# Kernel tuning notes

Hardware: AMD Instinct MI355X
Metric: run time of the kernel (lower is better)

The kernel has to match this reference:

```python
import jax, jax.numpy as jnp
import numpy as np
from jax import lax

B, S, H, T = 64, 512, 768, 9


def setup_inputs() -> dict:
    key = jax.random.key(0)
    ks = jax.random.split(key, 7)
    hidden = jax.random.normal(ks[0], (B, S, H), dtype=jnp.float32)
    W = jax.random.normal(ks[1], (H, T), dtype=jnp.float32) * 0.02
    b = jax.random.normal(ks[2], (T,), dtype=jnp.float32) * 0.02
    start_trans = jax.random.normal(ks[3], (T,), dtype=jnp.float32) * 0.1
    end_trans = jax.random.normal(ks[4], (T,), dtype=jnp.float32) * 0.1
    trans = jax.random.normal(ks[5], (T, T), dtype=jnp.float32) * 0.1
    labels = jax.random.randint(ks[6], (B, S), 0, T, dtype=jnp.int64)
    return {"hidden": hidden, "W": W, "b": b, "start_trans": start_trans,
            "end_trans": end_trans, "trans": trans, "labels": labels}


def _crf_nll(emissions, labels, start_trans, end_trans, trans):
    # emissions: [B,S,T], labels: [B,S] int. mask = labels > -1 (torchcrf semantics).
    maskf = (labels > -1).astype(emissions.dtype)          # [B,S]
    tags = jnp.maximum(labels, 0)                          # safe indexing

    # ---- numerator: score of the gold path ----
    tags0 = tags[:, 0]                                     # [B]
    num0 = start_trans[tags0] + jnp.take_along_axis(emissions[:, 0], tags0[:, None], axis=1)[:, 0]

    em_t = jnp.swapaxes(emissions[:, 1:], 0, 1)            # [S-1,B,T]
    tg_t = jnp.swapaxes(tags[:, 1:], 0, 1)                 # [S-1,B]
    mk_t = jnp.swapaxes(maskf[:, 1:], 0, 1)                # [S-1,B]

    def num_step(carry, xs):
        score, prev = carry
        em, tg, mk = xs
        step = trans[prev, tg] + jnp.take_along_axis(em, tg[:, None], axis=1)[:, 0]
        score = score + step * mk
        prev = jnp.where(mk > 0, tg, prev)
        return (score, prev), None

    (num, last_tags), _ = lax.scan(num_step, (num0, tags0), (em_t, tg_t, mk_t))
    num = num + end_trans[last_tags]                       # [B]

    # ---- denominator: log-partition via forward algorithm (log-semiring scan) ----
    alpha0 = start_trans[None, :] + emissions[:, 0]        # [B,T]

    def den_step(alpha, xs):
        em, mk = xs
        new = jax.nn.logsumexp(alpha[:, :, None] + trans[None, :, :], axis=1) + em  # [B,T]
        alpha = jnp.where(mk[:, None] > 0, new, alpha)
        return alpha, None

    alpha, _ = lax.scan(den_step, alpha0, (em_t, mk_t))
    den = jax.nn.logsumexp(alpha + end_trans[None, :], axis=1)  # [B]

    # model returns -crf(...) with reduction='mean'  =>  mean NLL
    return jnp.mean(den - num)


def reference(hidden, W, b, start_trans, end_trans, trans, labels):
    # token-classification head: [B,S,H] @ [H,T] -> emissions [B,S,T]
    emissions = jnp.einsum('bsh,ht->bst', hidden, W) + b
    return _crf_nll(emissions, labels, start_trans, end_trans, trans)
```

## Files before the change

kernel.cpp:

```cpp
#include <hip/hip_runtime.h>

constexpr int Bn = 64, Sn = 512, Hn = 768, Tn = 9;
constexpr int EMS = 12;
constexpr int CHUNKS = 32, CLEN = 16;

__device__ __forceinline__ float lse9(const float* e) {
    float m01 = fmaxf(e[0], e[1]), m23 = fmaxf(e[2], e[3]);
    float m45 = fmaxf(e[4], e[5]), m67 = fmaxf(e[6], e[7]);
    float m = fmaxf(fmaxf(fmaxf(m01, m23), fmaxf(m45, m67)), e[8]);
    float s = 0.f;
#pragma unroll
    for (int k = 0; k < 9; ++k) s += __expf(e[k] - m);
    return m + __logf(s);
}

__global__ __launch_bounds__(128) void fused_kernel(
        const float* __restrict__ hidden, const float* __restrict__ W,
        const float* __restrict__ bias, const float* __restrict__ trans,
        const int* __restrict__ labels,
        float* __restrict__ Mws, float* __restrict__ numpart,
        float* __restrict__ em0) {
    __shared__ float Wl[Hn * Tn];
    __shared__ float emch[CLEN][EMS];
    __shared__ float Mbuf[2][9][12];
    __shared__ int   labch[CLEN];

    const int b = blockIdx.x / CHUNKS;
    const int c = blockIdx.x % CHUNKS;
    const int tid = threadIdx.x;
    const int lane = tid & 63;
    const int wv = tid >> 6;

    const float4* Wg4 = reinterpret_cast<const float4*>(W);
    float4* Wl4 = reinterpret_cast<float4*>(Wl);
    for (int idx = tid; idx < Hn * Tn / 4; idx += 128) Wl4[idx] = Wg4[idx];
    if (tid < CLEN) labch[tid] = labels[b * Sn + c * CLEN + tid];
    float br[9];
#pragma unroll
    for (int t = 0; t < 9; ++t) br[t] = bias[t];
    __syncthreads();

    const size_t hbase = ((size_t)b * Sn + (size_t)c * CLEN) * Hn;
    const float4* hp0 = reinterpret_cast<const float4*>(hidden + hbase + (size_t)wv * Hn);
    float4 pre0 = hp0[lane], pre1 = hp0[lane + 64], pre2 = hp0[lane + 128];

    float wreg[3][36];
#pragma unroll
    for (int k = 0; k < 3; ++k) {
        const float4* p = reinterpret_cast<const float4*>(&Wl[(4 * lane + 256 * k) * Tn]);
#pragma unroll
        for (int j = 0; j < 9; ++j) {
            float4 q = p[j];
            wreg[k][4 * j + 0] = q.x; wreg[k][4 * j + 1] = q.y;
            wreg[k][4 * j + 2] = q.z; wreg[k][4 * j + 3] = q.w;
        }
    }

    for (int r = wv; r < CLEN; r += 2) {
        float4 v0 = pre0, v1 = pre1, v2 = pre2;
        if (r + 2 < CLEN) {
            const float4* hq = reinterpret_cast<const float4*>(hidden + hbase + (size_t)(r + 2) * Hn);
            pre0 = hq[lane]; pre1 = hq[lane + 64]; pre2 = hq[lane + 128];
        }
        const float hv[12] = {v0.x, v0.y, v0.z, v0.w, v1.x, v1.y, v1.z, v1.w,
                              v2.x, v2.y, v2.z, v2.w};
        float acc[9];
#pragma unroll
        for (int t = 0; t < 9; ++t) acc[t] = 0.f;
#pragma unroll
        for (int k = 0; k < 3; ++k)
#pragma unroll
            for (int cc = 0; cc < 4; ++cc)
#pragma unroll
                for (int t = 0; t < 9; ++t)
                    acc[t] = fmaf(hv[k * 4 + cc], wreg[k][cc * 9 + t], acc[t]);
#pragma unroll
        for (int m = 1; m < 64; m <<= 1)
#pragma unroll
            for (int t = 0; t < 9; ++t) acc[t] += __shfl_xor(acc[t], m, 64);
        if (lane == 0) {
#pragma unroll
            for (int t = 0; t < 9; ++t) emch[r][t] = acc[t] + br[t];
        }
    }
    __syncthreads();

    if (tid < 64) {
        float term = 0.f;
        if (tid < CLEN) {
            int sg = c * CLEN + tid;
            if (sg >= 1) {
                int l = labch[tid];
                if (l > -1) {
                    int lp = (tid > 0) ? labch[tid - 1] : labels[b * Sn + sg - 1];
                    if (lp < 0) lp = 0;
                    term = trans[lp * 9 + l] + emch[tid][l];
                }
            }
        }
#pragma unroll
        for (int m = 1; m < 16; m <<= 1) term += __shfl_xor(term, m, 64);
        if (tid == 0) numpart[b * CHUNKS + c] = term;
        if (c == 0 && tid < 9) em0[b * EMS + tid] = emch[0][tid];
    }

    const bool act = tid < 81;
    const int i = tid / 9, j = tid % 9;
    float tc[9], row[9];
    float nv = (i == j) ? 0.f : -1e30f;
    if (act) {
#pragma unroll
        for (int k = 0; k < 9; ++k) tc[k] = trans[k * 9 + j];
#pragma unroll
        for (int k = 0; k < 9; ++k) row[k] = (k == i) ? 0.f : -1e30f;
    }
    const int sbeg = (c == 0) ? 1 : 0;
    for (int sl = sbeg; sl < CLEN; ++sl) {
        if (act) {
            float e[9];
#pragma unroll
            for (int k = 0; k < 9; ++k) e[k] = row[k] + tc[k];
            float cand = lse9(e) + emch[sl][j];
            if (labch[sl] > -1) nv = cand;
            Mbuf[sl & 1][i][j] = nv;
        }
        __syncthreads();
        if (act) {
#pragma unroll
            for (int k = 0; k < 9; ++k) row[k] = Mbuf[sl & 1][i][k];
        }
    }
    if (act) Mws[(size_t)(b * CHUNKS + c) * 81 + tid] = nv;
}

__global__ __launch_bounds__(128) void final_kernel(
        const float* __restrict__ Mws, const float* __restrict__ numpart,
        const float* __restrict__ em0, const float* __restrict__ start,
        const float* __restrict__ endt, const int* __restrict__ labels,
        float* __restrict__ out) {
    const int b = blockIdx.x, tid = threadIdx.x;
    __shared__ float Ml[CHUNKS][9][12];
    __shared__ float nred;
    for (int idx = tid; idx < CHUNKS * 81; idx += 128) {
        int c = idx / 81, r = idx % 81;
        Ml[c][r / 9][r % 9] = Mws[(size_t)(b * CHUNKS + c) * 81 + r];
    }
    if (tid < 64) {
        float np = (tid < CHUNKS) ? numpart[b * CHUNKS + tid] : 0.f;
#pragma unroll
        for (int m = 1; m < 32; m <<= 1) np += __shfl_xor(np, m, 64);
        if (tid == 0) nred = np;
    }
    __syncthreads();
    if (tid < 9) {
        const int j = tid;
        float alpha[9];
#pragma unroll
        for (int k = 0; k < 9; ++k) alpha[k] = start[k] + em0[b * EMS + k];
        for (int c = 0; c < CHUNKS; ++c) {
            float e[9];
#pragma unroll
            for (int k = 0; k < 9; ++k) e[k] = alpha[k] + Ml[c][k][j];
            float nv = lse9(e);
#pragma unroll
            for (int k = 0; k < 9; ++k) alpha[k] = __shfl(nv, k, 64);
        }
        if (j == 0) {
            float e[9];
#pragma unroll
            for (int k = 0; k < 9; ++k) e[k] = alpha[k] + endt[k];
            float den = lse9(e);
            const int* lb = labels + b * Sn;
            int t0 = lb[0] > -1 ? lb[0] : 0;
            int lt = lb[Sn - 1] > -1 ? lb[Sn - 1] : 0;
            float num = nred + start[t0] + em0[b * EMS + t0] + endt[lt];
            atomicAdd(out, (den - num) * (1.0f / Bn));
        }
    }
}

extern "C" void kernel_launch(void* const* d_in, const int* in_sizes, int n_in,
                              void* d_out, int out_size, void* d_ws, size_t ws_size,
                              hipStream_t stream) {
    const float* hidden = (const float*)d_in[0];
    const float* W      = (const float*)d_in[1];
    const float* bias   = (const float*)d_in[2];
    const float* start  = (const float*)d_in[3];
    const float* endt   = (const float*)d_in[4];
    const float* trans  = (const float*)d_in[5];
    const int*   labels = (const int*)d_in[6];
    float* out = (float*)d_out;

    float* numpart = (float*)d_ws;
    float* em0     = numpart + Bn * CHUNKS;
    float* Mws     = em0 + Bn * EMS;

    hipMemsetAsync(d_out, 0, sizeof(float), stream);
    fused_kernel<<<Bn * CHUNKS, 128, 0, stream>>>(hidden, W, bias, trans, labels,
                                                  Mws, numpart, em0);
    final_kernel<<<Bn, 128, 0, stream>>>(Mws, numpart, em0, start, endt, labels, out);
}
```

Baseline: 195.2 us.

## Compute emission projection with bf16 MFMA instead of FP32 FMA and shuffles

Replaces the per-row FP32 dot product plus 64-lane shuffle reduction with a bf16 MFMA 16x16x32 tile. Each wave covers half of the hidden dimension for all 16 rows of the chunk, and the two partial results are summed through shared memory. W is stored transposed and padded in LDS so it can be loaded into B fragments, and launch bounds now request higher occupancy. The kernel is bound by reading hidden, so the gain may be limited. Rounding both hidden and W to bf16 lowers the precision of the emissions.

```diff
diff --git a/kernel.cpp b/kernel.cpp
--- a/kernel.cpp
+++ b/kernel.cpp
@@ -1,8 +1,18 @@
 #include <hip/hip_runtime.h>
+#include <hip/hip_bf16.h>
 
 constexpr int Bn = 64, Sn = 512, Hn = 768, Tn = 9;
 constexpr int EMS = 12;
 constexpr int CHUNKS = 32, CLEN = 16;
+constexpr int WPAD = 776;
+
+typedef __attribute__((ext_vector_type(8))) short bf16x8;
+typedef __attribute__((ext_vector_type(4))) float f32x4;
+
+__device__ __forceinline__ short f2bf(float x) {
+    __hip_bfloat16 h = __float2bfloat16(x);
+    return *reinterpret_cast<short*>(&h);
+}
 
 __device__ __forceinline__ float lse9(const float* e) {
     float m01 = fmaxf(e[0], e[1]), m23 = fmaxf(e[2], e[3]);
@@ -14,74 +24,63 @@
     return m + __logf(s);
 }
 
-__global__ __launch_bounds__(128) void fused_kernel(
+__global__ __launch_bounds__(128, 4) void fused_kernel(
         const float* __restrict__ hidden, const float* __restrict__ W,
         const float* __restrict__ bias, const float* __restrict__ trans,
         const int* __restrict__ labels,
         float* __restrict__ Mws, float* __restrict__ numpart,
         float* __restrict__ em0) {
-    __shared__ float Wl[Hn * Tn];
+    __shared__ float Wt[Tn * WPAD];
     __shared__ float emch[CLEN][EMS];
+    __shared__ f32x4 acc1[64];
     __shared__ float Mbuf[2][9][12];
-    __shared__ int   labch[CLEN];
+    __shared__ int   labch[CLEN + 1];
 
-    const int b = blockIdx.x / CHUNKS;
-    const int c = blockIdx.x % CHUNKS;
-    const int tid = threadIdx.x;
-    const int lane = tid & 63;
-    const int wv = tid >> 6;
+    const int b = blockIdx.x / CHUNKS, c = blockIdx.x % CHUNKS;
+    const int tid = threadIdx.x, lane = tid & 63, wv = tid >> 6;
 
-    const float4* Wg4 = reinterpret_cast<const float4*>(W);
-    float4* Wl4 = reinterpret_cast<float4*>(Wl);
-    for (int idx = tid; idx < Hn * Tn / 4; idx += 128) Wl4[idx] = Wg4[idx];
-    if (tid < CLEN) labch[tid] = labels[b * Sn + c * CLEN + tid];
-    float br[9];
-#pragma unroll
-    for (int t = 0; t < 9; ++t) br[t] = bias[t];
+    for (int f = tid; f < Hn * Tn; f += 128) {
+        int h = f / 9, t = f - 9 * h;
+        Wt[t * WPAD + h] = W[f];
+    }
+    if (tid < CLEN) labch[1 + tid] = labels[b * Sn + c * CLEN + tid];
+    if (tid == CLEN) labch[0] = (c > 0) ? labels[b * Sn + c * CLEN - 1] : 0;
     __syncthreads();
 
-    const size_t hbase = ((size_t)b * Sn + (size_t)c * CLEN) * Hn;
-    const float4* hp0 = reinterpret_cast<const float4*>(hidden + hbase + (size_t)wv * Hn);
-    float4 pre0 = hp0[lane], pre1 = hp0[lane + 64], pre2 = hp0[lane + 128];
+    const int c16 = lane & 15, hi = lane >> 4;
+    const bool on = c16 < Tn;
 
-    float wreg[3][36];
+    bf16x8 bfrag[12];
 #pragma unroll
-    for (int k = 0; k < 3; ++k) {
-        const float4* p = reinterpret_cast<const float4*>(&Wl[(4 * lane + 256 * k) * Tn]);
+    for (int mm = 0; mm < 12; ++mm) {
+        bf16x8 bf;
 #pragma unroll
-        for (int j = 0; j < 9; ++j) {
-            float4 q = p[j];
-            wreg[k][4 * j + 0] = q.x; wreg[k][4 * j + 1] = q.y;
-            wreg[k][4 * j + 2] = q.z; wreg[k][4 * j + 3] = q.w;
+        for (int e = 0; e < 8; ++e) {
+            float w = on ? Wt[c16 * WPAD + wv * 384 + 32 * mm + hi * 8 + e] : 0.f;
+            bf[e] = f2bf(w);
         }
+        bfrag[mm] = bf;
     }
 
-    for (int r = wv; r < CLEN; r += 2) {
-        float4 v0 = pre0, v1 = pre1, v2 = pre2;
-        if (r + 2 < CLEN) {
-            const float4* hq = reinterpret_cast<const float4*>(hidden + hbase + (size_t)(r + 2) * Hn);
-            pre0 = hq[lane]; pre1 = hq[lane + 64]; pre2 = hq[lane + 128];
-        }
-        const float hv[12] = {v0.x, v0.y, v0.z, v0.w, v1.x, v1.y, v1.z, v1.w,
-                              v2.x, v2.y, v2.z, v2.w};
-        float acc[9];
+    const float* abase = hidden + ((size_t)b * Sn + c * CLEN + c16) * Hn
+                                + wv * 384 + hi * 8;
+    f32x4 acc = {0.f, 0.f, 0.f, 0.f};
 #pragma unroll
-        for (int t = 0; t < 9; ++t) acc[t] = 0.f;
+    for (int mm = 0; mm < 12; ++mm) {
+        float4 u0 = *reinterpret_cast<const float4*>(abase + 32 * mm);
+        float4 u1 = *reinterpret_cast<const float4*>(abase + 32 * mm + 4);
+        bf16x8 af;
+        af[0] = f2bf(u0.x); af[1] = f2bf(u0.y); af[2] = f2bf(u0.z); af[3] = f2bf(u0.w);
+        af[4] = f2bf(u1.x); af[5] = f2bf(u1.y); af[6] = f2bf(u1.z); af[7] = f2bf(u1.w);
+        acc = __builtin_amdgcn_mfma_f32_16x16x32_bf16(af, bfrag[mm], acc, 0, 0, 0);
+    }
+    if (wv == 1) acc1[lane] = acc;
+    __syncthreads();
+    if (wv == 0 && on) {
+        f32x4 a1 = acc1[lane];
+        const float bcol = bias[c16];
 #pragma unroll
-        for (int k = 0; k < 3; ++k)
-#pragma unroll
-            for (int cc = 0; cc < 4; ++cc)
-#pragma unroll
-                for (int t = 0; t < 9; ++t)
-                    acc[t] = fmaf(hv[k * 4 + cc], wreg[k][cc * 9 + t], acc[t]);
-#pragma unroll
-        for (int m = 1; m < 64; m <<= 1)
-#pragma unroll
-            for (int t = 0; t < 9; ++t) acc[t] += __shfl_xor(acc[t], m, 64);
-        if (lane == 0) {
-#pragma unroll
-            for (int t = 0; t < 9; ++t) emch[r][t] = acc[t] + br[t];
-        }
+        for (int i = 0; i < 4; ++i) emch[hi * 4 + i][c16] = acc[i] + a1[i] + bcol;
     }
     __syncthreads();
 
@@ -89,20 +88,17 @@
         float term = 0.f;
         if (tid < CLEN) {
             int sg = c * CLEN + tid;
-            if (sg >= 1) {
-                int l = labch[tid];
-                if (l > -1) {
-                    int lp = (tid > 0) ? labch[tid - 1] : labels[b * Sn + sg - 1];
-                    if (lp < 0) lp = 0;
-                    term = trans[lp * 9 + l] + emch[tid][l];
-                }
+            int l = labch[1 + tid];
+            if (sg >= 1 && l > -1) {
+                int lp = labch[tid]; if (lp < 0) lp = 0;
+                term = trans[lp * 9 + l] + emch[tid][l];
             }
         }
 #pragma unroll
         for (int m = 1; m < 16; m <<= 1) term += __shfl_xor(term, m, 64);
         if (tid == 0) numpart[b * CHUNKS + c] = term;
-        if (c == 0 && tid < 9) em0[b * EMS + tid] = emch[0][tid];
     }
+    if (c == 0 && tid >= 64 && tid < 73) em0[b * EMS + (tid - 64)] = emch[0][tid - 64];
 
     const bool act = tid < 81;
     const int i = tid / 9, j = tid % 9;
@@ -114,6 +110,7 @@
 #pragma unroll
         for (int k = 0; k < 9; ++k) row[k] = (k == i) ? 0.f : -1e30f;
     }
+    __syncthreads();
     const int sbeg = (c == 0) ? 1 : 0;
     for (int sl = sbeg; sl < CLEN; ++sl) {
         if (act) {
@@ -121,7 +118,7 @@
 #pragma unroll
             for (int k = 0; k < 9; ++k) e[k] = row[k] + tc[k];
             float cand = lse9(e) + emch[sl][j];
-            if (labch[sl] > -1) nv = cand;
+            if (labch[1 + sl] > -1) nv = cand;
             Mbuf[sl & 1][i][j] = nv;
         }
         __syncthreads();
```

Result: slower. 199.6 us (+2.2%).
